# Performance work log

Measured on AMD Instinct MI355X. Metric: run time of the kernel, lower is better.

The kernel has to match this reference:

```python
import jax, jax.numpy as jnp
import numpy as np

THEA = 0.5
DELTA = 1.5
IGNORE = 255
K = 19  # num classes (len(weights))
LOSS_WEIGHT = 1.0
MIN_PIXELS = 20.0  # class kept only if pixel count > 20
WEIGHTS = jnp.ones((K,), dtype=jnp.float32)
EPS = 1e-12


def setup_inputs() -> dict:
    key = jax.random.key(0)
    k1, k2 = jax.random.split(key)
    n, c, h, w = 4, 32, 512, 1024
    predict = jax.random.normal(k1, (n, c, h, w), dtype=jnp.float32)
    target = jax.random.randint(k2, (n, h, w), 0, K, dtype=jnp.int32)
    return {"predict": predict, "target": target}


def _loss(predict, target):
    n, c, h, w = predict.shape
    # (n,c,h,w) -> (n*h*w, c), matching predict.permute(0,2,3,1)
    feat = jnp.transpose(predict, (0, 2, 3, 1)).reshape(-1, c)
    seg = target.reshape(-1)
    valid_pix = seg != IGNORE
    seg = jnp.where(valid_pix, seg, K).astype(jnp.int32)  # ignored -> extra segment K
    ones = valid_pix.astype(feat.dtype)

    # per-class counts and means (segment reduce replaces the python class loop)
    counts = jax.ops.segment_sum(ones, seg, num_segments=K + 1)[:K]
    sums = jax.ops.segment_sum(feat * ones[:, None], seg, num_segments=K + 1)[:K]
    centers = sums / jnp.maximum(counts, 1.0)[:, None]  # [K, c]
    valid_cls = counts > MIN_PIXELS
    n_cls = jnp.maximum(jnp.sum(valid_cls.astype(feat.dtype)), 1.0)

    # ---- variance term: relu(||mean - x|| - thea)^2, normalized by #positives ----
    ctr_ext = jnp.concatenate([centers, jnp.zeros((1, c), centers.dtype)], axis=0)
    ctr_pix = ctr_ext[seg]  # gather per-pixel center
    res = jnp.sqrt(jnp.sum((ctr_pix - feat) ** 2, axis=1) + EPS)  # [n*h*w]
    r = jax.nn.relu(res - THEA) * ones
    sq = jax.ops.segment_sum(r * r, seg, num_segments=K + 1)[:K]
    pos = jax.ops.segment_sum((r > 0).astype(feat.dtype), seg, num_segments=K + 1)[:K]
    norml = jnp.maximum(jax.lax.stop_gradient(pos), 1.0)  # numpy count in original: no grad
    loss_var = jnp.sum(jnp.where(valid_cls, WEIGHTS * sq / norml, 0.0)) / n_cls

    # ---- pairwise center distance term ----
    diff = centers[:, None, :] - centers[None, :, :]  # [K, K, c]
    dist = jnp.sqrt(jnp.sum(diff * diff, axis=-1) + EPS)
    pair_mask = valid_cls[:, None] & valid_cls[None, :] & ~jnp.eye(K, dtype=bool)
    d = jax.nn.relu(2.0 * DELTA - dist)
    loss_dis = jnp.sum(jnp.where(pair_mask, d * d, 0.0)) / jnp.maximum(n_cls * (n_cls - 1.0), 1.0)

    # ---- regularization term ----
    loss_reg = jnp.sum(jnp.where(valid_cls, jnp.sqrt(jnp.sum(centers * centers, axis=1) + EPS), 0.0)) / n_cls

    return LOSS_WEIGHT * (loss_var + loss_dis + 0.001 * loss_reg)


def reference(predict, target):
    return _loss(predict, target)
```

## Files before the change

### kernel.cpp

```cpp
#include <hip/hip_runtime.h>


#define K_CLS 19
#define C_CH 32
#define HW_SHIFT 19
#define HW_SIZE (1 << HW_SHIFT)
#define EPSF 1e-12f
#define THEA_F 0.5f
#define TWO_DELTA 3.0f
#define MIN_PIX 20.0f

#define OFF_PSUM 0
#define OFF_PCNT 40960
#define OFF_RED  42240
#define OFF_VRED 42880
#define OFF_VPART 42944
#define OFF_MAP  108480
#define WS_FLOATS (OFF_MAP + 524288)

typedef float __attribute__((ext_vector_type(4))) fx4;

__device__ __forceinline__ void atomAddF(float* p, float v) {
  unsafeAtomicAdd(p, v);
}

__device__ __forceinline__ float bperm(float v, int byteidx) {
  return __int_as_float(__builtin_amdgcn_ds_bpermute(byteidx, __float_as_int(v)));
}

__device__ __forceinline__ float4 ldnt4(const float* p) {
  const fx4 v = __builtin_nontemporal_load(reinterpret_cast<const fx4*>(p));
  return make_float4(v.x, v.y, v.z, v.w);
}

__global__ __launch_bounds__(256) void k_pack(
    const int* __restrict__ tgt, float* __restrict__ ws)
{
  const int i = blockIdx.x * 256 + threadIdx.x;
  const int4 c = *reinterpret_cast<const int4*>(tgt + (size_t)i * 4);
  const unsigned u = (unsigned)(c.x & 255) | ((unsigned)(c.y & 255) << 8)
                   | ((unsigned)(c.z & 255) << 16) | ((unsigned)(c.w & 255) << 24);
  reinterpret_cast<unsigned*>(ws + OFF_MAP)[i] = u;
}

__global__ __launch_bounds__(256) void k_accum(
    const float* __restrict__ pred, float* __restrict__ ws)
{
  __shared__ float sA[4][K_CLS][64];
  __shared__ float s_w[4][20];
  const int t = threadIdx.x;
  const int w = t >> 6;
  const int lane = t & 63;
  const unsigned* umap = reinterpret_cast<const unsigned*>(ws + OFF_MAP);
  float* colA = &sA[w][0][lane];
#pragma unroll
  for (int k = 0; k < K_CLS; ++k) colA[k << 6] = 0.f;

  if (blockIdx.x < 2048) {
    const int plane = blockIdx.x >> 4;
    const int slab  = blockIdx.x & 15;
    const int n_idx = plane >> 5;
    const int ch    = plane & 31;
    const float* pbase = pred + (((size_t)plane) << HW_SHIFT) + ((size_t)slab << 15);
    const int mbase = ((n_idx << HW_SHIFT) + (slab << 15)) >> 2;

    float4 vA = ldnt4(pbase + t * 4);
    unsigned mA = umap[mbase + t];
#pragma unroll 1
    for (int it = 0; it < 32; ++it) {
      float4 vB; unsigned mB;
      if (it + 1 < 32) {
        vB = ldnt4(pbase + (it + 1) * 1024 + t * 4);
        mB = umap[mbase + (it + 1) * 256 + t];
      }
      const unsigned b0 = mA & 255u, b1 = (mA >> 8) & 255u;
      const unsigned b2 = (mA >> 16) & 255u, b3 = mA >> 24;
      const int   k0 = min(b0, 18u), k1 = min(b1, 18u);
      const int   k2 = min(b2, 18u), k3 = min(b3, 18u);
      const float v0 = (b0 < K_CLS) ? vA.x : 0.f;
      const float v1 = (b1 < K_CLS) ? vA.y : 0.f;
      const float v2 = (b2 < K_CLS) ? vA.z : 0.f;
      const float v3 = (b3 < K_CLS) ? vA.w : 0.f;
      colA[k0 << 6] += v0;
      colA[k1 << 6] += v1;
      colA[k2 << 6] += v2;
      colA[k3 << 6] += v3;
      vA = vB; mA = mB;
    }

    float acc[K_CLS];
#pragma unroll
    for (int k = 0; k < K_CLS; ++k) acc[k] = colA[k << 6];
#pragma unroll
    for (int k = 0; k < K_CLS; ++k) {
      float s = acc[k];
#pragma unroll
      for (int m = 1; m < 64; m <<= 1) s += __shfl_xor(s, m, 64);
      acc[k] = s;
    }
#pragma unroll
    for (int k = 0; k < K_CLS; ++k)
      if (lane == k) s_w[w][k] = acc[k];
    __syncthreads();
    if (t < K_CLS) {
      const int slot = n_idx * 16 + slab;
      ws[OFF_PSUM + ch * (64 * 20) + slot * 20 + t] =
          s_w[0][t] + s_w[1][t] + s_w[2][t] + s_w[3][t];
    }
  } else {
    const int idx = blockIdx.x - 2048;
    const int mbase = idx << 13;

#pragma unroll 1
    for (int it = 0; it < 32; ++it) {
      const unsigned m = umap[mbase + it * 256 + t];
      const unsigned b0 = m & 255u, b1 = (m >> 8) & 255u;
      const unsigned b2 = (m >> 16) & 255u, b3 = m >> 24;
      colA[min(b0, 18u) << 6] += (b0 < K_CLS) ? 1.f : 0.f;
      colA[min(b1, 18u) << 6] += (b1 < K_CLS) ? 1.f : 0.f;
      colA[min(b2, 18u) << 6] += (b2 < K_CLS) ? 1.f : 0.f;
      colA[min(b3, 18u) << 6] += (b3 < K_CLS) ? 1.f : 0.f;
    }

    float acc[K_CLS];
#pragma unroll
    for (int k = 0; k < K_CLS; ++k) acc[k] = colA[k << 6];
#pragma unroll
    for (int k = 0; k < K_CLS; ++k) {
      float s = acc[k];
#pragma unroll
      for (int m = 1; m < 64; m <<= 1) s += __shfl_xor(s, m, 64);
      acc[k] = s;
    }
#pragma unroll
    for (int k = 0; k < K_CLS; ++k)
      if (lane == k) s_w[w][k] = acc[k];
    __syncthreads();
    if (t < K_CLS) {
      const int slot = idx;
      ws[OFF_PCNT + slot * 20 + t] = s_w[0][t] + s_w[1][t] + s_w[2][t] + s_w[3][t];
    }
  }
}

__global__ __launch_bounds__(64) void k_reduce(float* __restrict__ ws)
{
  const int o = blockIdx.x;
  const int lane = threadIdx.x;
  float a;
  if (o < C_CH * K_CLS) {
    const int ch = o / K_CLS, k = o - ch * K_CLS;
    a = ws[OFF_PSUM + ch * (64 * 20) + lane * 20 + k];
  } else {
    a = ws[OFF_PCNT + lane * 20 + (o - C_CH * K_CLS)];
  }
#pragma unroll
  for (int m = 1; m < 64; m <<= 1) a += __shfl_xor(a, m, 64);
  if (lane == 0) ws[OFF_RED + o] = a;
}

__global__ __launch_bounds__(256) void k_var(
    const float* __restrict__ pred, const int* __restrict__ tgt,
    float* __restrict__ ws)
{
  __shared__ float s_red[640];
  __shared__ float s_w[4][40];
  const int t = threadIdx.x;
  const int w = t >> 6;
  const int lane = t & 63;

  for (int i = t; i < 627; i += 256) s_red[i] = ws[OFF_RED + i];
  __syncthreads();

  const float invc = (lane < K_CLS) ? 1.f / fmaxf(s_red[608 + lane], 1.f) : 0.f;
  float ctrreg[C_CH];
  float c2reg = 0.f;
#pragma unroll
  for (int c = 0; c < C_CH; ++c) {
    ctrreg[c] = (lane < K_CLS) ? s_red[c * K_CLS + lane] * invc : 0.f;
    c2reg = fmaf(ctrreg[c], ctrreg[c], c2reg);
  }

  const int bpx = blockIdx.x * 2048;
  const int n_idx = bpx >> HW_SHIFT;
  const int hw0 = bpx & (HW_SIZE - 1);

  const int* tb = tgt + (((size_t)n_idx) << HW_SHIFT) + hw0;
  const int4 ca = *reinterpret_cast<const int4*>(tb + t * 4);
  const int4 cb = *reinterpret_cast<const int4*>(tb + 1024 + t * 4);
  const int cls[8] = {ca.x, ca.y, ca.z, ca.w, cb.x, cb.y, cb.z, cb.w};
  int idx8[8];
#pragma unroll
  for (int j = 0; j < 8; ++j)
    idx8[j] = min((unsigned)cls[j], 19u) << 2;

  float nrm[8] = {0.f,0.f,0.f,0.f,0.f,0.f,0.f,0.f};
  float dot[8] = {0.f,0.f,0.f,0.f,0.f,0.f,0.f,0.f};
#pragma unroll
  for (int c = 0; c < C_CH; ++c) {
    const float* cp = pred + (((size_t)(n_idx * C_CH + c)) << HW_SHIFT) + hw0;
    const float4 xa = ldnt4(cp + t * 4);
    const float4 xb = ldnt4(cp + 1024 + t * 4);
    const float x[8] = {xa.x, xa.y, xa.z, xa.w, xb.x, xb.y, xb.z, xb.w};
#pragma unroll
    for (int j = 0; j < 8; ++j) {
      const float cv = bperm(ctrreg[c], idx8[j]);
      nrm[j] = fmaf(x[j], x[j], nrm[j]);
      dot[j] = fmaf(x[j], cv, dot[j]);
    }
  }

  float acc_sq[K_CLS], acc_pos[K_CLS];
#pragma unroll
  for (int k = 0; k < K_CLS; ++k) { acc_sq[k] = 0.f; acc_pos[k] = 0.f; }
#pragma unroll
  for (int j = 0; j < 8; ++j) {
    const float c2j = bperm(c2reg, idx8[j]);
    const float d2 = fmaxf(nrm[j] - 2.f * dot[j] + c2j, 0.f);
    const float r = sqrtf(d2 + EPSF) - THEA_F;
    const bool act = ((unsigned)cls[j] < K_CLS) && (r > 0.f);
    const float rr = act ? r * r : 0.f;
    const float pp = act ? 1.f : 0.f;
    const int sc = min((unsigned)cls[j], 18u);
#pragma unroll
    for (int k = 0; k < K_CLS; ++k) {
      const bool b = (sc == k);
      acc_sq[k]  += b ? rr : 0.f;
      acc_pos[k] += b ? pp : 0.f;
    }
  }

#pragma unroll
  for (int k = 0; k < K_CLS; ++k) {
    float a = acc_sq[k], b = acc_pos[k];
#pragma unroll
    for (int m = 1; m < 64; m <<= 1) {
      a += __shfl_xor(a, m, 64);
      b += __shfl_xor(b, m, 64);
    }
    acc_sq[k] = a; acc_pos[k] = b;
  }
#pragma unroll
  for (int k = 0; k < K_CLS; ++k)
    if (lane == k) { s_w[w][k] = acc_sq[k]; s_w[w][20 + k] = acc_pos[k]; }
  __syncthreads();
  if (t < K_CLS) {
    float* vp = ws + OFF_VPART + (size_t)blockIdx.x * 64;
    vp[t]         = s_w[0][t] + s_w[1][t] + s_w[2][t] + s_w[3][t];
    vp[K_CLS + t] = s_w[0][20 + t] + s_w[1][20 + t] + s_w[2][20 + t] + s_w[3][20 + t];
  }
}

__global__ __launch_bounds__(256) void k_vred(float* __restrict__ ws)
{
  const int o = blockIdx.x;
  const int t = threadIdx.x;
  float a = 0.f;
#pragma unroll
  for (int r = 0; r < 4; ++r)
    a += ws[OFF_VPART + (size_t)(t + r * 256) * 64 + o];
#pragma unroll
  for (int m = 1; m < 64; m <<= 1) a += __shfl_xor(a, m, 64);
  __shared__ float s[4];
  if ((t & 63) == 0) s[t >> 6] = a;
  __syncthreads();
  if (t == 0) ws[OFF_VRED + o] = s[0] + s[1] + s[2] + s[3];
}

__global__ __launch_bounds__(1024) void k_final(
    float* __restrict__ ws, float* __restrict__ out)
{
  __shared__ float s_ctr[C_CH * K_CLS];
  __shared__ float s_valid[K_CLS];
  __shared__ float s_red[3];
  __shared__ float s_ncls;
  const int t = threadIdx.x;
  if (t < 3) s_red[t] = 0.f;
  if (t < K_CLS) s_valid[t] = (ws[OFF_RED + C_CH * K_CLS + t] > MIN_PIX) ? 1.f : 0.f;
  for (int i = t; i < C_CH * K_CLS; i += 1024) {
    const int k = i % K_CLS;
    s_ctr[i] = ws[OFF_RED + i] / fmaxf(ws[OFF_RED + C_CH * K_CLS + k], 1.f);
  }
  __syncthreads();

  if (t == 0) {
    float n = 0.f;
    for (int k = 0; k < K_CLS; ++k) n += s_valid[k];
    s_ncls = fmaxf(n, 1.f);
  }
  if (t < K_CLS && s_valid[t] > 0.f) {
    const float sq  = ws[OFF_VRED + t];
    const float pos = ws[OFF_VRED + K_CLS + t];
    atomAddF(&s_red[0], sq / fmaxf(pos, 1.f));
    float nn = 0.f;
#pragma unroll
    for (int ch = 0; ch < C_CH; ++ch) {
      const float cv = s_ctr[ch * K_CLS + t];
      nn = fmaf(cv, cv, nn);
    }
    atomAddF(&s_red[2], sqrtf(nn + EPSF));
  }
  if (t < K_CLS * K_CLS) {
    const int a = t / K_CLS, b = t - (t / K_CLS) * K_CLS;
    if (a != b && s_valid[a] > 0.f && s_valid[b] > 0.f) {
      float dd = 0.f;
#pragma unroll
      for (int ch = 0; ch < C_CH; ++ch) {
        const float df = s_ctr[ch * K_CLS + a] - s_ctr[ch * K_CLS + b];
        dd = fmaf(df, df, dd);
      }
      const float dist = sqrtf(dd + EPSF);
      const float d = fmaxf(TWO_DELTA - dist, 0.f);
      if (d > 0.f) atomAddF(&s_red[1], d * d);
    }
  }
  __syncthreads();
  if (t == 0) {
    const float n = s_ncls;
    out[0] = s_red[0] / n
           + s_red[1] / fmaxf(n * (n - 1.f), 1.f)
           + 0.001f * s_red[2] / n;
  }
}

extern "C" void kernel_launch(void* const* d_in, const int* in_sizes, int n_in,
                              void* d_out, int out_size, void* d_ws, size_t ws_size,
                              hipStream_t stream) {
  const float* pred = (const float*)d_in[0];
  const int*   tgt  = (const int*)d_in[1];
  float* ws  = (float*)d_ws;
  float* out = (float*)d_out;
  const int P = in_sizes[1];

  k_pack  <<<P / 1024, 256, 0, stream>>>(tgt, ws);
  k_accum <<<2048 + 64, 256, 0, stream>>>(pred, ws);
  k_reduce<<<C_CH * K_CLS + K_CLS, 64, 0, stream>>>(ws);
  k_var   <<<P / 2048, 256, 0, stream>>>(pred, tgt, ws);
  k_vred  <<<2 * K_CLS, 256, 0, stream>>>(ws);
  k_final <<<1, 1024, 0, stream>>>(ws, out);
}
```

Before: 419.4 us.

## Stash fp16 copy of predictions in accumulation pass for variance pass

While the first pass streams the fp32 prediction tensor, it also writes an fp16 copy into workspace. The variance pass then reads that half-size copy and the packed byte labels instead of re-reading fp32 predictions and int32 targets. This halves the bytes read in the second pass at the cost of an extra write in the first pass, and it introduces fp16 rounding of the features in the distance computation.

```diff
diff --git a/kernel.cpp b/kernel.cpp
--- a/kernel.cpp
+++ b/kernel.cpp
@@ -1,4 +1,5 @@
 #include <hip/hip_runtime.h>
+#include <hip/hip_fp16.h>
 
 
 #define K_CLS 19
@@ -16,7 +17,8 @@
 #define OFF_VRED 42880
 #define OFF_VPART 42944
 #define OFF_MAP  108480
-#define WS_FLOATS (OFF_MAP + 524288)
+#define OFF_STASH 655360
+#define WS_FLOATS (OFF_STASH + 33554432)
 
 typedef float __attribute__((ext_vector_type(4))) fx4;
 
@@ -31,6 +33,11 @@
 __device__ __forceinline__ float4 ldnt4(const float* p) {
   const fx4 v = __builtin_nontemporal_load(reinterpret_cast<const fx4*>(p));
   return make_float4(v.x, v.y, v.z, v.w);
+}
+
+__device__ __forceinline__ unsigned pkh2(float a, float b) {
+  __half2 h = __floats2half2_rn(a, b);
+  return *reinterpret_cast<unsigned*>(&h);
 }
 
 __global__ __launch_bounds__(256) void k_pack(
@@ -52,6 +59,7 @@
   const int w = t >> 6;
   const int lane = t & 63;
   const unsigned* umap = reinterpret_cast<const unsigned*>(ws + OFF_MAP);
+  unsigned* stash = reinterpret_cast<unsigned*>(ws + OFF_STASH);
   float* colA = &sA[w][0][lane];
 #pragma unroll
   for (int k = 0; k < K_CLS; ++k) colA[k << 6] = 0.f;
@@ -63,6 +71,7 @@
     const int ch    = plane & 31;
     const float* pbase = pred + (((size_t)plane) << HW_SHIFT) + ((size_t)slab << 15);
     const int mbase = ((n_idx << HW_SHIFT) + (slab << 15)) >> 2;
+    const size_t sbase = ((size_t)plane << 18) + ((size_t)slab << 14);
 
     float4 vA = ldnt4(pbase + t * 4);
     unsigned mA = umap[mbase + t];
@@ -73,6 +82,9 @@
         vB = ldnt4(pbase + (it + 1) * 1024 + t * 4);
         mB = umap[mbase + (it + 1) * 256 + t];
       }
+      *reinterpret_cast<uint2*>(stash + sbase + it * 512 + t * 2) =
+          make_uint2(pkh2(vA.x, vA.y), pkh2(vA.z, vA.w));
+
       const unsigned b0 = mA & 255u, b1 = (mA >> 8) & 255u;
       const unsigned b2 = (mA >> 16) & 255u, b3 = mA >> 24;
       const int   k0 = min(b0, 18u), k1 = min(b1, 18u);
@@ -160,14 +172,15 @@
 }
 
 __global__ __launch_bounds__(256) void k_var(
-    const float* __restrict__ pred, const int* __restrict__ tgt,
-    float* __restrict__ ws)
+    const float* __restrict__ pred, float* __restrict__ ws)
 {
   __shared__ float s_red[640];
   __shared__ float s_w[4][40];
   const int t = threadIdx.x;
   const int w = t >> 6;
   const int lane = t & 63;
+  const unsigned* umap = reinterpret_cast<const unsigned*>(ws + OFF_MAP);
+  const unsigned* stash = reinterpret_cast<const unsigned*>(ws + OFF_STASH);
 
   for (int i = t; i < 627; i += 256) s_red[i] = ws[OFF_RED + i];
   __syncthreads();
@@ -183,25 +196,37 @@
 
   const int bpx = blockIdx.x * 2048;
   const int n_idx = bpx >> HW_SHIFT;
-  const int hw0 = bpx & (HW_SIZE - 1);
-
-  const int* tb = tgt + (((size_t)n_idx) << HW_SHIFT) + hw0;
-  const int4 ca = *reinterpret_cast<const int4*>(tb + t * 4);
-  const int4 cb = *reinterpret_cast<const int4*>(tb + 1024 + t * 4);
-  const int cls[8] = {ca.x, ca.y, ca.z, ca.w, cb.x, cb.y, cb.z, cb.w};
+  const int hw0 = (bpx & (HW_SIZE - 1)) + t * 8;
+
+  const uint2 mw = *reinterpret_cast<const uint2*>(
+      umap + ((n_idx << HW_SHIFT) >> 2) + (hw0 >> 2));
+  unsigned cls[8];
+  cls[0] = mw.x & 255u; cls[1] = (mw.x >> 8) & 255u;
+  cls[2] = (mw.x >> 16) & 255u; cls[3] = mw.x >> 24;
+  cls[4] = mw.y & 255u; cls[5] = (mw.y >> 8) & 255u;
+  cls[6] = (mw.y >> 16) & 255u; cls[7] = mw.y >> 24;
   int idx8[8];
 #pragma unroll
   for (int j = 0; j < 8; ++j)
-    idx8[j] = min((unsigned)cls[j], 19u) << 2;
+    idx8[j] = (int)min(cls[j], 19u) << 2;
 
   float nrm[8] = {0.f,0.f,0.f,0.f,0.f,0.f,0.f,0.f};
   float dot[8] = {0.f,0.f,0.f,0.f,0.f,0.f,0.f,0.f};
 #pragma unroll
   for (int c = 0; c < C_CH; ++c) {
-    const float* cp = pred + (((size_t)(n_idx * C_CH + c)) << HW_SHIFT) + hw0;
-    const float4 xa = ldnt4(cp + t * 4);
-    const float4 xb = ldnt4(cp + 1024 + t * 4);
-    const float x[8] = {xa.x, xa.y, xa.z, xa.w, xb.x, xb.y, xb.z, xb.w};
+    const size_t swidx = (((size_t)(n_idx * C_CH + c)) << 18) + (hw0 >> 1);
+    const uint4 sv = *reinterpret_cast<const uint4*>(stash + swidx);
+    float x[8];
+    {
+      __half2 h0 = *reinterpret_cast<const __half2*>(&sv.x);
+      __half2 h1 = *reinterpret_cast<const __half2*>(&sv.y);
+      __half2 h2 = *reinterpret_cast<const __half2*>(&sv.z);
+      __half2 h3 = *reinterpret_cast<const __half2*>(&sv.w);
+      const float2 f0 = __half22float2(h0), f1 = __half22float2(h1);
+      const float2 f2 = __half22float2(h2), f3 = __half22float2(h3);
+      x[0] = f0.x; x[1] = f0.y; x[2] = f1.x; x[3] = f1.y;
+      x[4] = f2.x; x[5] = f2.y; x[6] = f3.x; x[7] = f3.y;
+    }
 #pragma unroll
     for (int j = 0; j < 8; ++j) {
       const float cv = bperm(ctrreg[c], idx8[j]);
@@ -218,10 +243,10 @@
     const float c2j = bperm(c2reg, idx8[j]);
     const float d2 = fmaxf(nrm[j] - 2.f * dot[j] + c2j, 0.f);
     const float r = sqrtf(d2 + EPSF) - THEA_F;
-    const bool act = ((unsigned)cls[j] < K_CLS) && (r > 0.f);
+    const bool act = (cls[j] < K_CLS) && (r > 0.f);
     const float rr = act ? r * r : 0.f;
     const float pp = act ? 1.f : 0.f;
-    const int sc = min((unsigned)cls[j], 18u);
+    const int sc = (int)min(cls[j], 18u);
 #pragma unroll
     for (int k = 0; k < K_CLS; ++k) {
       const bool b = (sc == k);
@@ -335,7 +360,7 @@
   k_pack  <<<P / 1024, 256, 0, stream>>>(tgt, ws);
   k_accum <<<2048 + 64, 256, 0, stream>>>(pred, ws);
   k_reduce<<<C_CH * K_CLS + K_CLS, 64, 0, stream>>>(ws);
-  k_var   <<<P / 2048, 256, 0, stream>>>(pred, tgt, ws);
+  k_var   <<<P / 2048, 256, 0, stream>>>(pred, ws);
   k_vred  <<<2 * K_CLS, 256, 0, stream>>>(ws);
   k_final <<<1, 1024, 0, stream>>>(ws, out);
 }
```

After: 431.1 us. +2.8%, slower.
